# Kernel tuning notes

Measured on AMD Instinct MI355X. Metric: run time of the kernel, lower is better.

Reference implementation:

```python
import jax, jax.numpy as jnp
from jax import lax
import numpy as np

# Config mirroring CSABlock(embed_dim=128, bs=8, heads=8, img_size=512, depth=2)
E = 128
BATCH = 8
HEADS = 8
RESO = 512 // 8      # 64
DEPTH = 2
SPLIT = 2            # split_size
C = 2 * E            # token dim = 256
C2 = C // 2          # per-branch dim
NH = HEADS // 2      # heads per branch
HID = 4 * C          # mlp hidden (mlp_ratio=4)
EPS = 1e-5


def setup_inputs() -> dict:
    key = jax.random.key(0)
    ks = iter(jax.random.split(key, 24))
    rn = lambda s, sd=0.02: jax.random.normal(next(ks), s, jnp.float32) * sd
    return {
        "x1": jax.random.normal(next(ks), (BATCH, E, RESO, RESO), jnp.float32),
        "x2": jax.random.normal(next(ks), (BATCH, E, RESO, RESO), jnp.float32),
        # conv_embed: Conv2d(C,C,3,1,1) + BatchNorm (eval) + LayerNorm
        "conv_w": rn((C, C, 3, 3)), "conv_b": jnp.zeros((C,), jnp.float32),
        "bn_g": jnp.ones((C,), jnp.float32), "bn_b": jnp.zeros((C,), jnp.float32),
        "bn_m": rn((C,), 0.1), "bn_v": jax.random.uniform(next(ks), (C,), jnp.float32) + 0.5,
        "ln0_g": jnp.ones((C,), jnp.float32), "ln0_b": jnp.zeros((C,), jnp.float32),
        # per-CSWinBlock params, stacked over DEPTH
        "n1_g": jnp.ones((DEPTH, C), jnp.float32), "n1_b": jnp.zeros((DEPTH, C), jnp.float32),
        "qkv_w": rn((DEPTH, C, 3 * C)),                       # Linear(dim, 3*dim, bias=False)
        "lepe_w": rn((DEPTH, 2, C2, 1, 3, 3)),                # depthwise get_v conv per branch
        "lepe_b": jnp.zeros((DEPTH, 2, C2), jnp.float32),
        "proj_w": rn((DEPTH, C, C)), "proj_b": jnp.zeros((DEPTH, C), jnp.float32),
        "n2_g": jnp.ones((DEPTH, C), jnp.float32), "n2_b": jnp.zeros((DEPTH, C), jnp.float32),
        "fc1_w": rn((DEPTH, C, HID)), "fc1_b": jnp.zeros((DEPTH, HID), jnp.float32),
        "fc2_w": rn((DEPTH, HID, C)), "fc2_b": jnp.zeros((DEPTH, C), jnp.float32),
    }


def _ln(x, g, b):
    mu = jnp.mean(x, -1, keepdims=True)
    var = jnp.mean((x - mu) ** 2, -1, keepdims=True)
    return (x - mu) * lax.rsqrt(var + EPS) * g + b


def _branch(q, k, v, Hs, Ws, dw_w, dw_b):
    """LePEAttention: cross-shaped stripe window attention with locally-enhanced PE.
    q,k,v: (B, L, C2); stripes of size Hs x Ws over a RESO x RESO grid."""
    B, L, c2 = q.shape
    H = W = RESO
    hd = c2 // NH
    scale = hd ** -0.5

    def to_win(t):  # (B,L,c2) -> (B*nW, NH, Hs*Ws, hd)
        t = t.reshape(B, H // Hs, Hs, W // Ws, Ws, c2)
        t = t.transpose(0, 1, 3, 2, 4, 5).reshape(-1, Hs * Ws, NH, hd)
        return t.transpose(0, 2, 1, 3)

    qw, kw = to_win(q), to_win(k)
    # v as per-window images for the depthwise LePE conv (padding is per-window)
    vimg = v.reshape(B, H // Hs, Hs, W // Ws, Ws, c2).transpose(0, 1, 3, 5, 2, 4)
    vimg = vimg.reshape(-1, c2, Hs, Ws)
    lepe = lax.conv_general_dilated(vimg, dw_w, (1, 1), [(1, 1), (1, 1)],
                                    dimension_numbers=("NCHW", "OIHW", "NCHW"),
                                    feature_group_count=c2) + dw_b[:, None, None]
    heads = lambda t: t.reshape(-1, NH, hd, Hs * Ws).transpose(0, 1, 3, 2)
    vw, lepe = heads(vimg), heads(lepe)

    attn = jax.nn.softmax(jnp.einsum("wnsd,wntd->wnst", qw * scale, kw), axis=-1)
    o = jnp.einsum("wnst,wntd->wnsd", attn, vw) + lepe      # (B*nW, NH, S, hd)
    # windows2img
    o = o.transpose(0, 2, 1, 3).reshape(B, H // Hs, W // Ws, Hs, Ws, c2)
    o = o.transpose(0, 1, 3, 2, 4, 5).reshape(B, L, c2)
    return o


def _forward(x1, x2, conv_w, conv_b, bn_g, bn_b, bn_m, bn_v, ln0_g, ln0_b,
             n1_g, n1_b, qkv_w, lepe_w, lepe_b, proj_w, proj_b,
             n2_g, n2_b, fc1_w, fc1_b, fc2_w, fc2_b):
    B, _, H, W = x1.shape
    t = jnp.concatenate([x1, x2], 1)                                   # (B, C, H, W)
    t = lax.conv_general_dilated(t, conv_w, (1, 1), [(1, 1), (1, 1)],
                                 dimension_numbers=("NCHW", "OIHW", "NCHW")) + conv_b[:, None, None]
    # BatchNorm2d in eval mode (running stats)
    t = (t - bn_m[:, None, None]) * lax.rsqrt(bn_v + EPS)[:, None, None] * bn_g[:, None, None] + bn_b[:, None, None]
    t = t.reshape(B, C, H * W).transpose(0, 2, 1)                      # b c h w -> b (h w) c
    t = _ln(t, ln0_g, ln0_b)

    for i in range(DEPTH):  # CSWinBlock x DEPTH
        img = _ln(t, n1_g[i], n1_b[i])
        qkv = (img @ qkv_w[i]).reshape(B, -1, 3, C)
        q, k, v = qkv[..., 0, :], qkv[..., 1, :], qkv[..., 2, :]
        # branch 0: horizontal stripes (H_sp=RESO, W_sp=SPLIT); branch 1: vertical
        xa = _branch(q[..., :C2], k[..., :C2], v[..., :C2], RESO, SPLIT, lepe_w[i, 0], lepe_b[i, 0])
        xb = _branch(q[..., C2:], k[..., C2:], v[..., C2:], SPLIT, RESO, lepe_w[i, 1], lepe_b[i, 1])
        att = jnp.concatenate([xa, xb], -1) @ proj_w[i] + proj_b[i]
        t = t + att
        y = _ln(t, n2_g[i], n2_b[i])
        t = t + (jax.nn.gelu(y @ fc1_w[i] + fc1_b[i], approximate=False) @ fc2_w[i] + fc2_b[i])

    x = t.transpose(0, 2, 1).reshape(B, C, H, W)
    return x[:, :E], x[:, E:]


def reference(x1, x2, conv_w, conv_b, bn_g, bn_b, bn_m, bn_v, ln0_g, ln0_b,
              n1_g, n1_b, qkv_w, lepe_w, lepe_b, proj_w, proj_b,
              n2_g, n2_b, fc1_w, fc1_b, fc2_w, fc2_b):
    return _forward(x1, x2, conv_w, conv_b, bn_g, bn_b, bn_m, bn_v, ln0_g, ln0_b,
                    n1_g, n1_b, qkv_w, lepe_w, lepe_b, proj_w, proj_b,
                    n2_g, n2_b, fc1_w, fc1_b, fc2_w, fc2_b)
```

## Files before the change

### kernel.cpp

```cpp
#include <hip/hip_runtime.h>
#include <hip/hip_bf16.h>

#define EPSV 1e-5f

using s8v = __attribute__((ext_vector_type(8))) short;
using f4v = __attribute__((ext_vector_type(4))) float;

__device__ __forceinline__ float bf2f(ushort u){
  union { unsigned int i; float f; } x; x.i = ((unsigned int)u)<<16; return x.f;
}
__device__ __forceinline__ ushort f2bf(float f){
  union { float f; unsigned int i; } x; x.f = f;
  unsigned int r = x.i + 0x7FFFu + ((x.i>>16)&1u);
  return (ushort)(r>>16);
}
__device__ __forceinline__ float wsum(float s){
  #pragma unroll
  for (int m=1;m<64;m<<=1) s += __shfl_xor(s, m);
  return s;
}
__device__ __forceinline__ float gelu_f(float t){
  return 0.5f*t*(1.0f + erff(t*0.70710678118654752f));
}

__device__ __forceinline__ void gload16(const void* g, void* l){
  __builtin_amdgcn_global_load_lds((__attribute__((address_space(1))) void*)g,
                                   (__attribute__((address_space(3))) void*)l, 16, 0, 0);
}

__global__ __launch_bounds__(256) void repack_in_k(const float* __restrict__ x1,
                                                   const float* __restrict__ x2,
                                                   ushort* __restrict__ Xin){
  __shared__ ushort tile[256][66];
  const int y = blockIdx.x, b = blockIdx.y, tid = threadIdx.x;
  const int xl = tid & 63, cq = tid >> 6;
  for (int it=0; it<64; it++){
    int ci = it*4 + cq;
    float v;
    if (ci < 128) v = x1[(((long)b*128 + ci)*64 + y)*64 + xl];
    else          v = x2[(((long)b*128 + (ci-128))*64 + y)*64 + xl];
    tile[ci][xl] = f2bf(v);
  }
  __syncthreads();
  for (int x=0; x<64; x++){
    Xin[(((long)b*66 + (y+1))*66 + (x+1))*256 + tid] = tile[tid][x];
  }
}

__global__ void prep_k(const float* __restrict__ conv_w, const float* __restrict__ qkv_w,
                       const float* __restrict__ proj_w, const float* __restrict__ fc1_w,
                       const float* __restrict__ fc2_w, const float* __restrict__ conv_b,
                       const float* __restrict__ bn_g, const float* __restrict__ bn_b,
                       const float* __restrict__ bn_m, const float* __restrict__ bn_v,
                       ushort* __restrict__ Wc, ushort* __restrict__ Wq, ushort* __restrict__ Wp,
                       ushort* __restrict__ W1, ushort* __restrict__ W2,
                       float* __restrict__ scv, float* __restrict__ shv)
{
  const long total = 589824L + 393216 + 131072 + 524288 + 524288 + 256;
  for (long idx = (long)blockIdx.x*256 + threadIdx.x; idx < total; idx += (long)gridDim.x*256){
    long e = idx;
    if (e < 589824){
      int co = (int)(e / 2304), kk = (int)(e % 2304);
      int dd = kk >> 8, ci = kk & 255;
      Wc[e] = f2bf(conv_w[((long)(co*256 + ci))*9 + dd]);
      continue;
    }
    e -= 589824;
    if (e < 393216){
      int l = (int)(e / 196608), r = (int)(e % 196608);
      int k = r / 768, n = r % 768;
      Wq[(long)l*196608 + (long)n*256 + k] = f2bf(qkv_w[(long)l*196608 + r]);
      continue;
    }
    e -= 393216;
    if (e < 131072){
      int l = (int)(e / 65536), r = (int)(e % 65536);
      int k = r >> 8, n = r & 255;
      Wp[(long)l*65536 + n*256 + k] = f2bf(proj_w[(long)l*65536 + r]);
      continue;
    }
    e -= 131072;
    if (e < 524288){
      int l = (int)(e / 262144), r = (int)(e % 262144);
      int k = r >> 10, n = r & 1023;
      W1[(long)l*262144 + (long)n*256 + k] = f2bf(fc1_w[(long)l*262144 + r]);
      continue;
    }
    e -= 524288;
    if (e < 524288){
      int l = (int)(e / 262144), r = (int)(e % 262144);
      int k = r >> 8, n = r & 255;
      W2[(long)l*262144 + (long)n*1024 + k] = f2bf(fc2_w[(long)l*262144 + r]);
      continue;
    }
    e -= 524288;
    {
      int n = (int)e;
      float s = bn_g[n] * rsqrtf(bn_v[n] + EPSV);
      scv[n] = s;
      shv[n] = (conv_b[n] - bn_m[n])*s + bn_b[n];
    }
  }
}

__global__ __launch_bounds__(256) void gemm_conv(
    const ushort* __restrict__ Xin, const ushort* __restrict__ Wt,
    const float* __restrict__ sc, const float* __restrict__ sh,
    float* __restrict__ T, const float* __restrict__ g1, const float* __restrict__ b1,
    const float* __restrict__ g2, const float* __restrict__ b2,
    ushort* __restrict__ Xb)
{
  const int K = 2304;
  __shared__ ushort SMEM[40960];
  const int tid = threadIdx.x, wid = tid>>6, lane = tid&63;
  const int m0 = blockIdx.x*64;
  const int l15 = lane&15, lg = lane>>4;
  const int rS = wid*8 + (lane>>3);
  const int cS = (((lane&7) ^ (lane>>3))*8);

  const ushort* pA[2];
  #pragma unroll
  for (int j=0;j<2;j++){
    int t = m0 + j*32 + rS;
    int b = t>>12, y = (t>>6)&63, x = t&63;
    pA[j] = Xin + ((long)((b*66 + y+1)*66) + (x+1))*256 + cS;
  }
  const ushort* pB[8];
  #pragma unroll
  for (int j=0;j<8;j++) pB[j] = Wt + (long)(j*32 + rS)*K + cS;

  auto stage = [&](int buf, int k0){
    ushort* AsB = SMEM + buf*20480;
    ushort* BsB = AsB + 4096;
    int dd = k0 >> 8;
    int dy = dd/3, dx = dd - dy*3;
    int koffA = ((dy-1)*66 + (dx-1))*256 + (k0 & 255);
    #pragma unroll
    for (int j=0;j<2;j++)
      gload16(pA[j] + koffA, (void*)&AsB[(j*256 + wid*64)*8]);
    #pragma unroll
    for (int j=0;j<8;j++)
      gload16(pB[j] + k0, (void*)&BsB[(j*256 + wid*64)*8]);
  };

  f4v acc[4][4] = {};

  int cur = 0;
  stage(0, 0);
  __syncthreads();
  for (int k0=0; k0<K; k0+=64){
    if (k0 + 64 < K) stage(cur^1, k0 + 64);
    const ushort* AsB = SMEM + cur*20480;
    const ushort* BsB = AsB + 4096;
    #pragma unroll
    for (int kk=0; kk<2; kk++){
      s8v a[4], b[4];
      const int kch = ((kk*4 + lg) ^ (l15 & 7))*8;
      #pragma unroll
      for (int mi=0;mi<4;mi++) a[mi] = *(const s8v*)&AsB[(mi*16 + l15)*64 + kch];
      #pragma unroll
      for (int ni=0;ni<4;ni++) b[ni] = *(const s8v*)&BsB[(wid*64 + ni*16 + l15)*64 + kch];
      #pragma unroll
      for (int mi=0;mi<4;mi++)
        #pragma unroll
        for (int ni=0;ni<4;ni++)
          acc[mi][ni] = __builtin_amdgcn_mfma_f32_16x16x32_bf16(a[mi], b[ni], acc[mi][ni], 0,0,0);
    }
    __syncthreads();
    cur ^= 1;
  }

  float* CT = (float*)SMEM;
  #pragma unroll
  for (int mi=0;mi<4;mi++)
    #pragma unroll
    for (int ni=0;ni<4;ni++)
      #pragma unroll
      for (int r=0;r<4;r++)
        CT[(mi*16 + lg*4 + r)*256 + wid*64 + ni*16 + l15] = acc[mi][ni][r];
  __syncthreads();

  const int c0 = lane*4;
  const float4 scv4 = *(const float4*)&sc[c0], shv4 = *(const float4*)&sh[c0];
  const float4 g1v = *(const float4*)&g1[c0], b1v = *(const float4*)&b1[c0];
  const float4 g2v = *(const float4*)&g2[c0], b2v = *(const float4*)&b2[c0];

  for (int t=0; t<16; t++){
    const int r = wid*16 + t;
    const long gmr = m0 + r;
    float4 v = *(float4*)&CT[r*256 + c0];
    float4 t4;
    t4.x = v.x*scv4.x + shv4.x; t4.y = v.y*scv4.y + shv4.y;
    t4.z = v.z*scv4.z + shv4.z; t4.w = v.w*scv4.w + shv4.w;
    float mu = wsum(t4.x+t4.y+t4.z+t4.w) * (1.0f/256.0f);
    float d0=t4.x-mu, d1=t4.y-mu, d2=t4.z-mu, d3=t4.w-mu;
    float rs = rsqrtf(wsum(d0*d0+d1*d1+d2*d2+d3*d3)*(1.0f/256.0f) + EPSV);
    float u0 = d0*rs*g1v.x + b1v.x, u1 = d1*rs*g1v.y + b1v.y;
    float u2 = d2*rs*g1v.z + b1v.z, u3 = d3*rs*g1v.w + b1v.w;
    float4 u = {u0,u1,u2,u3};
    *(float4*)&T[gmr*256 + c0] = u;
    float mu2 = wsum(u0+u1+u2+u3) * (1.0f/256.0f);
    float e0=u0-mu2, e1=u1-mu2, e2=u2-mu2, e3=u3-mu2;
    float rs2 = rsqrtf(wsum(e0*e0+e1*e1+e2*e2+e3*e3)*(1.0f/256.0f) + EPSV);
    ushort4 o; o.x=f2bf(e0*rs2*g2v.x + b2v.x); o.y=f2bf(e1*rs2*g2v.y + b2v.y);
    o.z=f2bf(e2*rs2*g2v.z + b2v.z); o.w=f2bf(e3*rs2*g2v.w + b2v.w);
    *(ushort4*)&Xb[gmr*256 + c0] = o;
  }
}

template<int EPI>
__global__ __launch_bounds__(256) void gemm_res(
    const ushort* __restrict__ A, const ushort* __restrict__ Wt, const float* __restrict__ bias,
    float* __restrict__ T, const float* __restrict__ g1, const float* __restrict__ b1,
    ushort* __restrict__ Xb, float* __restrict__ dout, int K)
{
  __shared__ ushort SMEM[20480];
  ushort* As = SMEM;
  ushort* Bs = SMEM + 4096;
  const int tid = threadIdx.x, wid = tid>>6, lane = tid&63;
  const int m0 = blockIdx.x*64;
  const int l15 = lane&15, lg = lane>>4;
  const int rS = wid*8 + (lane>>3);
  const int cS = (((lane&7) ^ (lane>>3))*8);

  const ushort* pA[2];
  #pragma unroll
  for (int j=0;j<2;j++) pA[j] = A + (long)(m0 + j*32 + rS)*K + cS;
  const ushort* pB[8];
  #pragma unroll
  for (int j=0;j<8;j++) pB[j] = Wt + (long)(j*32 + rS)*K + cS;

  f4v acc[4][4] = {};

  for (int k0=0; k0<K; k0+=64){
    #pragma unroll
    for (int j=0;j<2;j++)
      gload16(pA[j] + k0, (void*)&As[(j*256 + wid*64)*8]);
    #pragma unroll
    for (int j=0;j<8;j++)
      gload16(pB[j] + k0, (void*)&Bs[(j*256 + wid*64)*8]);
    __syncthreads();
    #pragma unroll
    for (int kk=0; kk<2; kk++){
      s8v a[4], b[4];
      const int kch = ((kk*4 + lg) ^ (l15 & 7))*8;
      #pragma unroll
      for (int mi=0;mi<4;mi++) a[mi] = *(const s8v*)&As[(mi*16 + l15)*64 + kch];
      #pragma unroll
      for (int ni=0;ni<4;ni++) b[ni] = *(const s8v*)&Bs[(wid*64 + ni*16 + l15)*64 + kch];
      #pragma unroll
      for (int mi=0;mi<4;mi++)
        #pragma unroll
        for (int ni=0;ni<4;ni++)
          acc[mi][ni] = __builtin_amdgcn_mfma_f32_16x16x32_bf16(a[mi], b[ni], acc[mi][ni], 0,0,0);
    }
    __syncthreads();
  }

  float* CT = (float*)SMEM;
  const int c0 = lane*4;
  const float4 bias4 = *(const float4*)&bias[c0];
  float4 g1v, b1v;
  if (EPI==1){ g1v = *(const float4*)&g1[c0]; b1v = *(const float4*)&b1[c0]; }
  const int b_ = m0>>12, y_ = (m0>>6)&63;

  #pragma unroll
  for (int p=0; p<2; p++){
    #pragma unroll
    for (int mi=2*p; mi<2*p+2; mi++)
      #pragma unroll
      for (int ni=0;ni<4;ni++)
        #pragma unroll
        for (int r=0;r<4;r++)
          CT[((mi-2*p)*16 + lg*4 + r)*256 + wid*64 + ni*16 + l15] = acc[mi][ni][r];
    __syncthreads();
    for (int t=0; t<8; t++){
      const int r = wid*8 + t;
      const long gmr = m0 + p*32 + r;
      float4 v = *(float4*)&CT[r*256 + c0];
      float4 rv = *(float4*)&T[gmr*256 + c0];
      float4 t4;
      t4.x = rv.x + v.x + bias4.x; t4.y = rv.y + v.y + bias4.y;
      t4.z = rv.z + v.z + bias4.z; t4.w = rv.w + v.w + bias4.w;
      if (EPI==3){
        *(float4*)&CT[r*256 + c0] = t4;
      } else {
        *(float4*)&T[gmr*256 + c0] = t4;
        float mu = wsum(t4.x+t4.y+t4.z+t4.w) * (1.0f/256.0f);
        float d0=t4.x-mu, d1=t4.y-mu, d2=t4.z-mu, d3=t4.w-mu;
        float rs = rsqrtf(wsum(d0*d0+d1*d1+d2*d2+d3*d3)*(1.0f/256.0f) + EPSV);
        ushort4 o; o.x=f2bf(d0*rs*g1v.x + b1v.x); o.y=f2bf(d1*rs*g1v.y + b1v.y);
        o.z=f2bf(d2*rs*g1v.z + b1v.z); o.w=f2bf(d3*rs*g1v.w + b1v.w);
        *(ushort4*)&Xb[gmr*256 + c0] = o;
      }
    }
    __syncthreads();
    if (EPI==3){
      float* obase = dout + (long)b_*524288 + (long)y_*64 + p*32;
      for (int it=0; it<32; it++){
        int e = it*256 + tid;
        int c = e>>5, xl = e&31;
        obase[(long)(c>>7)*4194304 + (long)(c&127)*4096 + xl] = CT[xl*256 + c];
      }
      __syncthreads();
    }
  }
}

#define BM 128
#define BN 128
#define BK 64
__global__ __launch_bounds__(256) void gemm_fc1(
    const ushort* __restrict__ A,
    const ushort* __restrict__ Wt, const float* __restrict__ bias,
    ushort* __restrict__ outb, int N, int K)
{
  __shared__ ushort SMEM[BM*BK + BN*BK];
  ushort* As = SMEM;
  ushort* Bs = SMEM + BM*BK;
  const int tid = threadIdx.x, wid = tid>>6, lane = tid&63;
  const int m0 = blockIdx.x*BM, n0 = blockIdx.y*BN;
  const int wm = (wid>>1)*64, wn = (wid&1)*64;
  const int l15 = lane&15, lg = lane>>4;

  const int rA = wid*32 + (lane>>3);
  const int cS = (((lane&7) ^ (lane>>3))*8);
  const ushort* pA[4];
  #pragma unroll
  for (int j=0;j<4;j++) pA[j] = A + (long)(m0 + rA + j*8)*K + cS;
  const ushort* pB[4];
  #pragma unroll
  for (int j=0;j<4;j++) pB[j] = Wt + (long)(n0 + rA + j*8)*K + cS;

  f4v acc[4][4] = {};

  for (int k0=0; k0<K; k0+=BK){
    #pragma unroll
    for (int j=0;j<4;j++){
      gload16(pA[j] + k0, (void*)&As[(wid*32 + j*8)*BK]);
      gload16(pB[j] + k0, (void*)&Bs[(wid*32 + j*8)*BK]);
    }
    __syncthreads();
    #pragma unroll
    for (int kk=0; kk<2; kk++){
      s8v a[4], b[4];
      const int kch = ((kk*4 + lg) ^ (l15 & 7))*8;
      #pragma unroll
      for (int mi=0;mi<4;mi++) a[mi] = *(const s8v*)&As[(wm + mi*16 + l15)*BK + kch];
      #pragma unroll
      for (int ni=0;ni<4;ni++) b[ni] = *(const s8v*)&Bs[(wn + ni*16 + l15)*BK + kch];
      #pragma unroll
      for (int mi=0;mi<4;mi++)
        #pragma unroll
        for (int ni=0;ni<4;ni++)
          acc[mi][ni] = __builtin_amdgcn_mfma_f32_16x16x32_bf16(a[mi], b[ni], acc[mi][ni], 0,0,0);
    }
    __syncthreads();
  }

  float* CT = (float*)SMEM;
  #pragma unroll
  for (int p=0; p<2; p++){
    if ((wid>>1) == p){
      #pragma unroll
      for (int mi=0;mi<4;mi++)
        #pragma unroll
        for (int ni=0;ni<4;ni++)
          #pragma unroll
          for (int r=0;r<4;r++)
            CT[(mi*16 + lg*4 + r)*128 + wn + ni*16 + l15] = acc[mi][ni][r];
    }
    __syncthreads();
    #pragma unroll
    for (int it=0; it<8; it++){
      int e = it*256 + tid;
      int row = e >> 5;
      int c4 = e & 31;
      float4 v = *(float4*)&CT[row*128 + c4*4];
      int gm = m0 + p*64 + row;
      int gn = n0 + c4*4;
      float4 bv = *(const float4*)&bias[gn];
      float t0 = gelu_f(v.x + bv.x), t1 = gelu_f(v.y + bv.y);
      float t2 = gelu_f(v.z + bv.z), t3 = gelu_f(v.w + bv.w);
      ushort4 u; u.x=f2bf(t0); u.y=f2bf(t1); u.z=f2bf(t2); u.w=f2bf(t3);
      *(ushort4*)&outb[(long)gm*N + gn] = u;
    }
    __syncthreads();
  }
}

__global__ __launch_bounds__(256) void gemm_qkv(
    const ushort* __restrict__ A,
    const ushort* __restrict__ Wt,
    ushort* __restrict__ outb, int K)
{
  __shared__ ushort SMEM[BM*BK + BN*BK];
  ushort* As = SMEM;
  ushort* Bs = SMEM + BM*BK;
  const int tid = threadIdx.x, wid = tid>>6, lane = tid&63;
  const int m0 = blockIdx.x*BM, n0 = blockIdx.y*BN;
  const int wm = (wid>>1)*64, wn = (wid&1)*64;
  const int l15 = lane&15, lg = lane>>4;

  const int rA = wid*32 + (lane>>3);
  const int cS = (((lane&7) ^ (lane>>3))*8);
  const ushort* pA[4];
  #pragma unroll
  for (int j=0;j<4;j++) pA[j] = A + (long)(m0 + rA + j*8)*K + cS;
  const ushort* pB[4];
  #pragma unroll
  for (int j=0;j<4;j++) pB[j] = Wt + (long)(n0 + rA + j*8)*K + cS;

  f4v acc[4][4] = {};

  for (int k0=0; k0<K; k0+=BK){
    #pragma unroll
    for (int j=0;j<4;j++){
      gload16(pA[j] + k0, (void*)&As[(wid*32 + j*8)*BK]);
      gload16(pB[j] + k0, (void*)&Bs[(wid*32 + j*8)*BK]);
    }
    __syncthreads();
    #pragma unroll
    for (int kk=0; kk<2; kk++){
      s8v a[4], b[4];
      const int kch = ((kk*4 + lg) ^ (l15 & 7))*8;
      #pragma unroll
      for (int mi=0;mi<4;mi++) a[mi] = *(const s8v*)&As[(wm + mi*16 + l15)*BK + kch];
      #pragma unroll
      for (int ni=0;ni<4;ni++) b[ni] = *(const s8v*)&Bs[(wn + ni*16 + l15)*BK + kch];
      #pragma unroll
      for (int mi=0;mi<4;mi++)
        #pragma unroll
        for (int ni=0;ni<4;ni++)
          acc[mi][ni] = __builtin_amdgcn_mfma_f32_16x16x32_bf16(a[mi], b[ni], acc[mi][ni], 0,0,0);
    }
    __syncthreads();
  }

  ushort* CB = SMEM;
  #pragma unroll
  for (int ni=0;ni<4;ni++){
    const int c = wn + ni*16 + l15;
    const int j = c>>3, ce = c&7;
    #pragma unroll
    for (int mi=0;mi<4;mi++)
      #pragma unroll
      for (int r=0;r<4;r++){
        const int row = wm + mi*16 + lg*4 + r;
        CB[row*128 + (((j ^ (row&7))<<3) | ce)] = f2bf(acc[mi][ni][r]);
      }
  }
  __syncthreads();

  const int tile = n0 >> 8;
  const int brq  = (n0 >> 7) & 1;
  const int b_   = m0 >> 12;
  const int Y0   = (m0 >> 6) & 63;
  if (brq == 0){
    #pragma unroll
    for (int it=0; it<8; it++){
      int g = it*256 + tid;
      int seg = g >> 4, q = g & 15;
      int h = seg >> 5, wv = seg & 31;
      int svi = q >> 2, c8 = q & 3;
      int gm_local = (svi>>1)*64 + wv*2 + (svi&1);
      int jc = h*4 + c8;
      uint4 v = *(uint4*)&CB[gm_local*128 + ((jc ^ (gm_local&7))<<3)];
      long rowb = ((long)(tile*2)*4 + h)*32768L + ((long)b_*32 + wv)*128 + (Y0*2 + svi);
      *(uint4*)&outb[rowb*32 + c8*8] = v;
    }
  } else {
    const int wv = Y0 >> 1;
    #pragma unroll
    for (int it=0; it<8; it++){
      int g = it*256 + tid;
      int h = g >> 9, rem = g & 511, sv = rem >> 2, c8 = rem & 3;
      int jc = h*4 + c8;
      uint4 v = *(uint4*)&CB[sv*128 + ((jc ^ (sv&7))<<3)];
      long rowb = ((long)(tile*2 + 1)*4 + h)*32768L + ((long)b_*32 + wv)*128 + sv;
      *(uint4*)&outb[rowb*32 + c8*8] = v;
    }
  }
}

__global__ __launch_bounds__(256) void attn_k(
    const ushort* __restrict__ QKVw, ushort* __restrict__ ATT,
    const float* __restrict__ lepe_w, const float* __restrict__ lepe_b, int layer)
{
  __shared__ ushort q_lds[128][36];
  __shared__ ushort k_lds[128][36];
  __shared__ ushort vT[32][132];
  __shared__ float wl[32][9];
  __shared__ float bl[32];
  const int tid = threadIdx.x, wid = tid>>6, lane = tid&63;
  const int b = blockIdx.y;
  const int br = blockIdx.z;
  const int w = blockIdx.x>>2, h = blockIdx.x&3;
  const int choff = br*128 + h*32;
  const int l15 = lane&15, lg = lane>>4;

  const long rowbase = ((long)b*32 + w)*128;
  const ushort* qb = QKVw + (((long)(0*2+br)*4 + h)*32768L + rowbase)*32;
  const ushort* kb = QKVw + (((long)(1*2+br)*4 + h)*32768L + rowbase)*32;
  const ushort* vb = QKVw + (((long)(2*2+br)*4 + h)*32768L + rowbase)*32;

  for (int e = tid; e < 512; e += 256){
    int row = e>>2, c4 = (e&3)*8;
    *(uint4*)&q_lds[row][c4] = *(const uint4*)(qb + (long)e*8);
    *(uint4*)&k_lds[row][c4] = *(const uint4*)(kb + (long)e*8);
    uint4 val = *(const uint4*)(vb + (long)e*8);
    const ushort* u = (const ushort*)&val;
    #pragma unroll
    for (int jj=0;jj<8;jj++) vT[c4+jj][row] = u[jj];
  }
  for (int e = tid; e < 288; e += 256){
    int d = e/9, tap = e%9;
    wl[d][tap] = lepe_w[((long)((layer*2+br)*128 + h*32 + d))*9 + tap];
  }
  if (tid < 32) bl[tid] = lepe_b[(layer*2+br)*128 + h*32 + tid];
  __syncthreads();

  const int wrow = wid*32;
  const float scale = 0.17677669529663689f;
  const int srcE = (lane & 15) | ((lane & 16) << 1);
  const int srcO = srcE + 16;
  const bool hi = (lane >= 32);
  const int HsL = (br==0)?64:2, WsL = (br==0)?2:64;

  #pragma unroll
  for (int mi=0; mi<2; mi++){
    s8v aq = *(const s8v*)&q_lds[wrow + mi*16 + l15][lg*8];
    f4v S[8];
    #pragma unroll
    for (int ni=0; ni<8; ni++){
      s8v bk = *(const s8v*)&k_lds[ni*16 + l15][lg*8];
      f4v z = {0.f,0.f,0.f,0.f};
      S[ni] = __builtin_amdgcn_mfma_f32_16x16x32_bf16(bk, aq, z, 0,0,0);
    }
    float mx = -1e30f;
    #pragma unroll
    for (int ni=0; ni<8; ni++)
      #pragma unroll
      for (int r=0;r<4;r++){ S[ni][r] *= scale; mx = fmaxf(mx, S[ni][r]); }
    mx = fmaxf(mx, __shfl_xor(mx, 16));
    mx = fmaxf(mx, __shfl_xor(mx, 32));
    float sum = 0.f;
    #pragma unroll
    for (int ni=0; ni<8; ni++)
      #pragma unroll
      for (int r=0;r<4;r++){ S[ni][r] = __expf(S[ni][r]-mx); sum += S[ni][r]; }
    sum += __shfl_xor(sum, 16);
    sum += __shfl_xor(sum, 32);
    const float inv = 1.0f / sum;
    unsigned int Alo[8], Ahi[8];
    #pragma unroll
    for (int ni=0; ni<8; ni++){
      Alo[ni] = (unsigned)f2bf(S[ni][0]*inv) | ((unsigned)f2bf(S[ni][1]*inv)<<16);
      Ahi[ni] = (unsigned)f2bf(S[ni][2]*inv) | ((unsigned)f2bf(S[ni][3]*inv)<<16);
    }
    f4v acc2[2] = {{0.f,0.f,0.f,0.f},{0.f,0.f,0.f,0.f}};
    #pragma unroll
    for (int ks=0; ks<4; ks++){
      unsigned e0 = (unsigned)__shfl((int)Alo[2*ks],   srcE);
      unsigned e1 = (unsigned)__shfl((int)Ahi[2*ks],   srcE);
      unsigned e2 = (unsigned)__shfl((int)Alo[2*ks+1], srcE);
      unsigned e3 = (unsigned)__shfl((int)Ahi[2*ks+1], srcE);
      unsigned o0 = (unsigned)__shfl((int)Alo[2*ks],   srcO);
      unsigned o1 = (unsigned)__shfl((int)Ahi[2*ks],   srcO);
      unsigned o2 = (unsigned)__shfl((int)Alo[2*ks+1], srcO);
      unsigned o3 = (unsigned)__shfl((int)Ahi[2*ks+1], srcO);
      union { unsigned u[4]; s8v v; } ap;
      ap.u[0] = hi?e2:e0; ap.u[1] = hi?e3:e1; ap.u[2] = hi?o2:o0; ap.u[3] = hi?o3:o1;
      #pragma unroll
      for (int di=0; di<2; di++){
        s8v bv = *(const s8v*)&vT[di*16 + l15][ks*32 + lg*8];
        acc2[di] = __builtin_amdgcn_mfma_f32_16x16x32_bf16(ap.v, bv, acc2[di], 0,0,0);
      }
    }
    #pragma unroll
    for (int di=0; di<2; di++)
      #pragma unroll
      for (int r=0;r<4;r++){
        int s = wrow + mi*16 + lg*4 + r;
        int d = di*16 + l15;
        float v = acc2[di][r] + bl[d];
        int hs, ws2;
        if (br==0){ hs = s>>1; ws2 = s&1; }
        else      { hs = s>>6; ws2 = s&63; }
        #pragma unroll
        for (int a=-1;a<=1;a++)
          #pragma unroll
          for (int bb=-1;bb<=1;bb++){
            int h2 = hs+a, w2 = ws2+bb;
            if (h2>=0 && h2<HsL && w2>=0 && w2<WsL){
              int s2 = h2*WsL + w2;
              v += wl[d][(a+1)*3 + (bb+1)] * bf2f(vT[d][s2]);
            }
          }
        int y, x;
        if (br==0){ y = s>>1; x = (w<<1)|(s&1); }
        else      { y = (w<<1)|(s>>6); x = s&63; }
        long tok = ((long)b*64 + y)*64 + x;
        ATT[tok*256 + choff + d] = f2bf(v);
      }
  }
}

extern "C" void kernel_launch(void* const* d_in, const int* in_sizes, int n_in,
                              void* d_out, int out_size, void* d_ws, size_t ws_size,
                              hipStream_t stream)
{
  (void)in_sizes; (void)n_in; (void)out_size;
  const float* x1     = (const float*)d_in[0];
  const float* x2     = (const float*)d_in[1];
  const float* conv_w = (const float*)d_in[2];
  const float* conv_b = (const float*)d_in[3];
  const float* bn_g   = (const float*)d_in[4];
  const float* bn_b   = (const float*)d_in[5];
  const float* bn_m   = (const float*)d_in[6];
  const float* bn_v   = (const float*)d_in[7];
  const float* ln0_g  = (const float*)d_in[8];
  const float* ln0_b  = (const float*)d_in[9];
  const float* n1_g   = (const float*)d_in[10];
  const float* n1_b   = (const float*)d_in[11];
  const float* qkv_w  = (const float*)d_in[12];
  const float* lepe_w = (const float*)d_in[13];
  const float* lepe_b = (const float*)d_in[14];
  const float* proj_w = (const float*)d_in[15];
  const float* proj_b = (const float*)d_in[16];
  const float* n2_g   = (const float*)d_in[17];
  const float* n2_b   = (const float*)d_in[18];
  const float* fc1_w  = (const float*)d_in[19];
  const float* fc1_b  = (const float*)d_in[20];
  const float* fc2_w  = (const float*)d_in[21];
  const float* fc2_b  = (const float*)d_in[22];

  if (ws_size < 121767936ULL){
    hipMemsetAsync(d_out, 0, (size_t)out_size*4, stream);
    return;
  }

  char* ws = (char*)d_ws;
  ushort* Xin  = (ushort*)ws;
  ushort* QKVb = (ushort*)ws;
  ushort* H1b  = (ushort*)ws;
  ushort* ATTb = (ushort*)(ws + 50331648);
  float*  T    = (float*)(ws + 67108864);
  ushort* Xb   = (ushort*)(ws + 100663296);
  size_t off = 117440512;
  ushort* Wc   = (ushort*)(ws + off); off += 1179648;
  ushort* Wq   = (ushort*)(ws + off); off += 786432;
  ushort* Wp   = (ushort*)(ws + off); off += 262144;
  ushort* W1   = (ushort*)(ws + off); off += 1048576;
  ushort* W2   = (ushort*)(ws + off); off += 1048576;
  float*  scv  = (float*)(ws + off);  off += 1024;
  float*  shv  = (float*)(ws + off);  off += 1024;

  hipMemsetAsync(Xin, 0, (size_t)8*66*66*256*2, stream);
  repack_in_k<<<dim3(64,8), 256, 0, stream>>>(x1, x2, Xin);
  prep_k<<<1024, 256, 0, stream>>>(conv_w, qkv_w, proj_w, fc1_w, fc2_w,
                                   conv_b, bn_g, bn_b, bn_m, bn_v,
                                   Wc, Wq, Wp, W1, W2, scv, shv);

  gemm_conv<<<512,256,0,stream>>>(Xin, Wc, scv, shv, T, ln0_g, ln0_b, n1_g, n1_b, Xb);

  for (int i=0;i<2;i++){
    gemm_qkv<<<dim3(256,6),256,0,stream>>>(Xb, Wq + (long)i*196608, QKVb, 256);
    attn_k<<<dim3(128,8,2),256,0,stream>>>(QKVb, ATTb, lepe_w, lepe_b, i);
    gemm_res<1><<<512,256,0,stream>>>(ATTb, Wp + (long)i*65536, proj_b + i*256,
                                      T, n2_g + i*256, n2_b + i*256, Xb, nullptr, 256);
    gemm_fc1<<<dim3(256,8),256,0,stream>>>(Xb, W1 + (long)i*262144, fc1_b + i*1024, H1b, 1024, 256);
    if (i == 0){
      gemm_res<1><<<512,256,0,stream>>>(H1b, W2, fc2_b,
                                        T, n1_g + 256, n1_b + 256, Xb, nullptr, 1024);
    } else {
      gemm_res<3><<<512,256,0,stream>>>(H1b, W2 + 262144, fc2_b + 256,
                                        T, nullptr, nullptr, nullptr, (float*)d_out, 1024);
    }
  }
}
```

Baseline: 446.0 us.

## Double-buffer LDS tiles with BK=32 in the three GEMM kernels

Rewrites the main loops of gemm_res, gemm_fc1 and gemm_qkv to use two LDS buffers with a K-step of 32. The next tile's async global-to-LDS loads are issued before the MFMA work on the current tile, so memory latency can overlap compute, and only one barrier per iteration is needed. The swizzle pattern is changed to match the 32-wide rows. In exchange, each k-step does half the MFMA work per barrier, which adds loop and synchronisation overhead per unit of compute.

```diff
diff --git a/kernel.cpp b/kernel.cpp
--- a/kernel.cpp
+++ b/kernel.cpp
@@ -215,46 +215,47 @@
     ushort* __restrict__ Xb, float* __restrict__ dout, int K)
 {
   __shared__ ushort SMEM[20480];
-  ushort* As = SMEM;
-  ushort* Bs = SMEM + 4096;
   const int tid = threadIdx.x, wid = tid>>6, lane = tid&63;
   const int m0 = blockIdx.x*64;
   const int l15 = lane&15, lg = lane>>4;
-  const int rS = wid*8 + (lane>>3);
-  const int cS = (((lane&7) ^ (lane>>3))*8);
-
-  const ushort* pA[2];
-  #pragma unroll
-  for (int j=0;j<2;j++) pA[j] = A + (long)(m0 + j*32 + rS)*K + cS;
-  const ushort* pB[8];
-  #pragma unroll
-  for (int j=0;j<8;j++) pB[j] = Wt + (long)(j*32 + rS)*K + cS;
+  const int rowS = wid*16 + (lane>>2);
+  const int cSrc = (((lane&3) ^ ((lane>>3)&3))*8);
+
+  const ushort* pA = A + (long)(m0 + rowS)*K + cSrc;
+  const ushort* pB[4];
+  #pragma unroll
+  for (int j=0;j<4;j++) pB[j] = Wt + (long)(j*64 + rowS)*K + cSrc;
+
+  auto stage = [&](int buf, int k0){
+    ushort* S = SMEM + buf*10240;
+    gload16(pA + k0, (void*)&S[tid*8]);
+    #pragma unroll
+    for (int j=0;j<4;j++)
+      gload16(pB[j] + k0, (void*)&S[2048 + j*2048 + tid*8]);
+  };
 
   f4v acc[4][4] = {};
 
-  for (int k0=0; k0<K; k0+=64){
-    #pragma unroll
-    for (int j=0;j<2;j++)
-      gload16(pA[j] + k0, (void*)&As[(j*256 + wid*64)*8]);
-    #pragma unroll
-    for (int j=0;j<8;j++)
-      gload16(pB[j] + k0, (void*)&Bs[(j*256 + wid*64)*8]);
-    __syncthreads();
-    #pragma unroll
-    for (int kk=0; kk<2; kk++){
-      s8v a[4], b[4];
-      const int kch = ((kk*4 + lg) ^ (l15 & 7))*8;
-      #pragma unroll
-      for (int mi=0;mi<4;mi++) a[mi] = *(const s8v*)&As[(mi*16 + l15)*64 + kch];
-      #pragma unroll
-      for (int ni=0;ni<4;ni++) b[ni] = *(const s8v*)&Bs[(wid*64 + ni*16 + l15)*64 + kch];
-      #pragma unroll
-      for (int mi=0;mi<4;mi++)
-        #pragma unroll
-        for (int ni=0;ni<4;ni++)
-          acc[mi][ni] = __builtin_amdgcn_mfma_f32_16x16x32_bf16(a[mi], b[ni], acc[mi][ni], 0,0,0);
-    }
-    __syncthreads();
+  int cur = 0;
+  stage(0, 0);
+  __syncthreads();
+  for (int k0=0; k0<K; k0+=32){
+    if (k0 + 32 < K) stage(cur^1, k0 + 32);
+    const ushort* As_ = SMEM + cur*10240;
+    const ushort* Bs_ = As_ + 2048;
+    const int kch = (lg ^ ((l15>>1)&3))*8;
+    s8v a[4], b[4];
+    #pragma unroll
+    for (int mi=0;mi<4;mi++) a[mi] = *(const s8v*)&As_[(mi*16 + l15)*32 + kch];
+    #pragma unroll
+    for (int ni=0;ni<4;ni++) b[ni] = *(const s8v*)&Bs_[(wid*64 + ni*16 + l15)*32 + kch];
+    #pragma unroll
+    for (int mi=0;mi<4;mi++)
+      #pragma unroll
+      for (int ni=0;ni<4;ni++)
+        acc[mi][ni] = __builtin_amdgcn_mfma_f32_16x16x32_bf16(a[mi], b[ni], acc[mi][ni], 0,0,0);
+    __syncthreads();
+    cur ^= 1;
   }
 
   float* CT = (float*)SMEM;
@@ -309,53 +310,58 @@
 
 #define BM 128
 #define BN 128
-#define BK 64
 __global__ __launch_bounds__(256) void gemm_fc1(
     const ushort* __restrict__ A,
     const ushort* __restrict__ Wt, const float* __restrict__ bias,
     ushort* __restrict__ outb, int N, int K)
 {
-  __shared__ ushort SMEM[BM*BK + BN*BK];
-  ushort* As = SMEM;
-  ushort* Bs = SMEM + BM*BK;
+  __shared__ ushort SMEM[16384];
   const int tid = threadIdx.x, wid = tid>>6, lane = tid&63;
   const int m0 = blockIdx.x*BM, n0 = blockIdx.y*BN;
   const int wm = (wid>>1)*64, wn = (wid&1)*64;
   const int l15 = lane&15, lg = lane>>4;
-
-  const int rA = wid*32 + (lane>>3);
-  const int cS = (((lane&7) ^ (lane>>3))*8);
-  const ushort* pA[4];
-  #pragma unroll
-  for (int j=0;j<4;j++) pA[j] = A + (long)(m0 + rA + j*8)*K + cS;
-  const ushort* pB[4];
-  #pragma unroll
-  for (int j=0;j<4;j++) pB[j] = Wt + (long)(n0 + rA + j*8)*K + cS;
+  const int rowS = wid*16 + (lane>>2);
+  const int cSrc = (((lane&3) ^ ((lane>>3)&3))*8);
+
+  const ushort* pA[2];
+  #pragma unroll
+  for (int j=0;j<2;j++) pA[j] = A + (long)(m0 + j*64 + rowS)*K + cSrc;
+  const ushort* pB[2];
+  #pragma unroll
+  for (int j=0;j<2;j++) pB[j] = Wt + (long)(n0 + j*64 + rowS)*K + cSrc;
+
+  auto stage = [&](int buf, int k0){
+    ushort* S = SMEM + buf*8192;
+    #pragma unroll
+    for (int j=0;j<2;j++)
+      gload16(pA[j] + k0, (void*)&S[j*2048 + tid*8]);
+    #pragma unroll
+    for (int j=0;j<2;j++)
+      gload16(pB[j] + k0, (void*)&S[4096 + j*2048 + tid*8]);
+  };
 
   f4v acc[4][4] = {};
 
-  for (int k0=0; k0<K; k0+=BK){
-    #pragma unroll
-    for (int j=0;j<4;j++){
-      gload16(pA[j] + k0, (void*)&As[(wid*32 + j*8)*BK]);
-      gload16(pB[j] + k0, (void*)&Bs[(wid*32 + j*8)*BK]);
-    }
-    __syncthreads();
-    #pragma unroll
-    for (int kk=0; kk<2; kk++){
-      s8v a[4], b[4];
-      const int kch = ((kk*4 + lg) ^ (l15 & 7))*8;
-      #pragma unroll
-      for (int mi=0;mi<4;mi++) a[mi] = *(const s8v*)&As[(wm + mi*16 + l15)*BK + kch];
-      #pragma unroll
-      for (int ni=0;ni<4;ni++) b[ni] = *(const s8v*)&Bs[(wn + ni*16 + l15)*BK + kch];
-      #pragma unroll
-      for (int mi=0;mi<4;mi++)
-        #pragma unroll
-        for (int ni=0;ni<4;ni++)
-          acc[mi][ni] = __builtin_amdgcn_mfma_f32_16x16x32_bf16(a[mi], b[ni], acc[mi][ni], 0,0,0);
-    }
-    __syncthreads();
+  int cur = 0;
+  stage(0, 0);
+  __syncthreads();
+  for (int k0=0; k0<K; k0+=32){
+    if (k0 + 32 < K) stage(cur^1, k0 + 32);
+    const ushort* As_ = SMEM + cur*8192;
+    const ushort* Bs_ = As_ + 4096;
+    const int kch = (lg ^ ((l15>>1)&3))*8;
+    s8v a[4], b[4];
+    #pragma unroll
+    for (int mi=0;mi<4;mi++) a[mi] = *(const s8v*)&As_[(wm + mi*16 + l15)*32 + kch];
+    #pragma unroll
+    for (int ni=0;ni<4;ni++) b[ni] = *(const s8v*)&Bs_[(wn + ni*16 + l15)*32 + kch];
+    #pragma unroll
+    for (int mi=0;mi<4;mi++)
+      #pragma unroll
+      for (int ni=0;ni<4;ni++)
+        acc[mi][ni] = __builtin_amdgcn_mfma_f32_16x16x32_bf16(a[mi], b[ni], acc[mi][ni], 0,0,0);
+    __syncthreads();
+    cur ^= 1;
   }
 
   float* CT = (float*)SMEM;
@@ -394,47 +400,53 @@
     const ushort* __restrict__ Wt,
     ushort* __restrict__ outb, int K)
 {
-  __shared__ ushort SMEM[BM*BK + BN*BK];
-  ushort* As = SMEM;
-  ushort* Bs = SMEM + BM*BK;
+  __shared__ ushort SMEM[16384];
   const int tid = threadIdx.x, wid = tid>>6, lane = tid&63;
   const int m0 = blockIdx.x*BM, n0 = blockIdx.y*BN;
   const int wm = (wid>>1)*64, wn = (wid&1)*64;
   const int l15 = lane&15, lg = lane>>4;
-
-  const int rA = wid*32 + (lane>>3);
-  const int cS = (((lane&7) ^ (lane>>3))*8);
-  const ushort* pA[4];
-  #pragma unroll
-  for (int j=0;j<4;j++) pA[j] = A + (long)(m0 + rA + j*8)*K + cS;
-  const ushort* pB[4];
-  #pragma unroll
-  for (int j=0;j<4;j++) pB[j] = Wt + (long)(n0 + rA + j*8)*K + cS;
+  const int rowS = wid*16 + (lane>>2);
+  const int cSrc = (((lane&3) ^ ((lane>>3)&3))*8);
+
+  const ushort* pA[2];
+  #pragma unroll
+  for (int j=0;j<2;j++) pA[j] = A + (long)(m0 + j*64 + rowS)*K + cSrc;
+  const ushort* pB[2];
+  #pragma unroll
+  for (int j=0;j<2;j++) pB[j] = Wt + (long)(n0 + j*64 + rowS)*K + cSrc;
+
+  auto stage = [&](int buf, int k0){
+    ushort* S = SMEM + buf*8192;
+    #pragma unroll
+    for (int j=0;j<2;j++)
+      gload16(pA[j] + k0, (void*)&S[j*2048 + tid*8]);
+    #pragma unroll
+    for (int j=0;j<2;j++)
+      gload16(pB[j] + k0, (void*)&S[4096 + j*2048 + tid*8]);
+  };
 
   f4v acc[4][4] = {};
 
-  for (int k0=0; k0<K; k0+=BK){
-    #pragma unroll
-    for (int j=0;j<4;j++){
-      gload16(pA[j] + k0, (void*)&As[(wid*32 + j*8)*BK]);
-      gload16(pB[j] + k0, (void*)&Bs[(wid*32 + j*8)*BK]);
-    }
-    __syncthreads();
-    #pragma unroll
-    for (int kk=0; kk<2; kk++){
-      s8v a[4], b[4];
-      const int kch = ((kk*4 + lg) ^ (l15 & 7))*8;
-      #pragma unroll
-      for (int mi=0;mi<4;mi++) a[mi] = *(const s8v*)&As[(wm + mi*16 + l15)*BK + kch];
-      #pragma unroll
-      for (int ni=0;ni<4;ni++) b[ni] = *(const s8v*)&Bs[(wn + ni*16 + l15)*BK + kch];
-      #pragma unroll
-      for (int mi=0;mi<4;mi++)
-        #pragma unroll
-        for (int ni=0;ni<4;ni++)
-          acc[mi][ni] = __builtin_amdgcn_mfma_f32_16x16x32_bf16(a[mi], b[ni], acc[mi][ni], 0,0,0);
-    }
-    __syncthreads();
+  int cur = 0;
+  stage(0, 0);
+  __syncthreads();
+  for (int k0=0; k0<K; k0+=32){
+    if (k0 + 32 < K) stage(cur^1, k0 + 32);
+    const ushort* As_ = SMEM + cur*8192;
+    const ushort* Bs_ = As_ + 4096;
+    const int kch = (lg ^ ((l15>>1)&3))*8;
+    s8v a[4], b[4];
+    #pragma unroll
+    for (int mi=0;mi<4;mi++) a[mi] = *(const s8v*)&As_[(wm + mi*16 + l15)*32 + kch];
+    #pragma unroll
+    for (int ni=0;ni<4;ni++) b[ni] = *(const s8v*)&Bs_[(wn + ni*16 + l15)*32 + kch];
+    #pragma unroll
+    for (int mi=0;mi<4;mi++)
+      #pragma unroll
+      for (int ni=0;ni<4;ni++)
+        acc[mi][ni] = __builtin_amdgcn_mfma_f32_16x16x32_bf16(a[mi], b[ni], acc[mi][ni], 0,0,0);
+    __syncthreads();
+    cur ^= 1;
   }
 
   ushort* CB = SMEM;
```

New measurement: 433.6 us, median of 2. -2.8%, faster.
